# Kernel optimization log

Hardware: AMD Instinct MI355X
Metric: run time of the kernel (lower is better)

## Reference

```python
import jax, jax.numpy as jnp
import numpy as np

ADMP = 8  # admp_channel -> K = ADMP*ADMP keypoints


def setup_inputs() -> dict:
    key = jax.random.key(0)
    kA, kB = jax.random.split(key)
    B, C, H, W = 8, 512, 96, 96
    feature_A = jax.random.normal(kA, (B, C, H, W), dtype=jnp.float32)
    feature_B = jax.random.normal(kB, (B, C, H, W), dtype=jnp.float32)
    return {"feature_A": feature_A, "feature_B": feature_B}


def _keypoint_rowcol(feature_A):
    # featureSelect: sum over channels, AdaptiveMaxPool2d(ADMP) with return_indices.
    # H,W divisible by ADMP so adaptive pool == uniform non-overlapping pooling.
    B, C, H, W = feature_A.shape
    ph, pw = H // ADMP, W // ADMP
    resp = feature_A.sum(axis=1)  # [B,H,W]
    r = resp.reshape(B, ADMP, ph, ADMP, pw).transpose(0, 1, 3, 2, 4)
    r = r.reshape(B, ADMP * ADMP, ph * pw)
    loc = jnp.argmax(r, axis=-1)  # first-max, matches torch  [B,K]
    kk = jnp.arange(ADMP * ADMP)
    gi, gj = kk // ADMP, kk % ADMP
    row_A = gi[None, :] * ph + loc // pw  # [B,K]
    col_A = gj[None, :] * pw + loc % pw
    return row_A, col_A


def reference(feature_A, feature_B):
    B, C, H, W = feature_A.shape
    K = ADMP * ADMP
    row_A, col_A = _keypoint_rowcol(feature_A)
    flat_A = row_A * W + col_A  # [B,K]

    # gather descriptors: [B,K,C]
    fa = feature_A.reshape(B, C, H * W)
    desc = jnp.take_along_axis(fa, flat_A[:, None, :], axis=2).transpose(0, 2, 1)

    # squared L2 distance map via ||b||^2 - 2 a.b + ||a||^2 : [B,K,HW]
    fb = feature_B.reshape(B, C, H * W)
    fb_sq = jnp.sum(fb * fb, axis=1)            # [B,HW]
    d_sq = jnp.sum(desc * desc, axis=-1)        # [B,K]
    cross = jnp.einsum('bkc,bcn->bkn', desc, fb)  # [B,K,HW]
    dist = fb_sq[:, None, :] - 2.0 * cross + d_sq[:, :, None]

    min_idx = jnp.argmin(dist, axis=-1)  # [B,K]
    row_B = min_idx // W
    col_B = min_idx % W
    drow = -(row_B - row_A)
    dcol = -(col_B - col_A)
    off = jnp.stack([drow, dcol], axis=-1)  # [B,K,2] int

    # getTranslationalOffsetByMode: most frequent (drow,dcol) pair per batch
    eq = jnp.all(off[:, :, None, :] == off[:, None, :, :], axis=-1)  # [B,K,K]
    counts = eq.sum(axis=-1)  # [B,K]
    best = jnp.argmax(counts, axis=-1)  # first occurrence on ties, matches dict order
    out = jnp.take_along_axis(off, best[:, None, None], axis=1)[:, 0, :]  # [B,2]
    return out
```

## Files before the change

### kernel.cpp

```cpp
#include <hip/hip_runtime.h>
#include <hip/hip_bf16.h>
#include <math.h>

typedef _Float16 half8 __attribute__((ext_vector_type(8)));
typedef __fp16 fp16x2 __attribute__((ext_vector_type(2)));
typedef float f32x4 __attribute__((ext_vector_type(4)));
typedef unsigned short u16x4 __attribute__((ext_vector_type(4)));
typedef unsigned short u16x8 __attribute__((ext_vector_type(8)));

#define B_   8
#define C_   512
#define H_   96
#define W_   96
#define HW   9216
#define K_   64
#define PH   12
#define PW   12
#define NT   96
#define CCH  32
#define NBLK 96

#define OFF_PARTIAL 0u
#define OFF_CANDV   0u
#define OFF_CANDN   294912u
#define OFF_DESCH   2359296u
#define OFF_DESCL   2883584u
#define OFF_ROWA    3407872u
#define OFF_COLA    3409920u

#define FBT_HI 0
#define FBT_LO 3072
#define DSC_HI 6144
#define DSC_LO 8704
#define BUFHW  11264

__global__ __launch_bounds__(256) void k_partial(const float* __restrict__ A,
                                                 float* __restrict__ part) {
    int idx4 = blockIdx.x * 256 + threadIdx.x;
    int chunk = blockIdx.y;
    int b = idx4 / (HW / 4), hw4 = idx4 - b * (HW / 4);
    const float* p = A + ((size_t)(b * C_ + chunk * 64)) * HW + hw4 * 4;
    float4 s = make_float4(0.f, 0.f, 0.f, 0.f);
#pragma unroll
    for (int i = 0; i < 64; ++i) {
        float4 v = *(const float4*)&p[(size_t)i * HW];
        s.x += v.x; s.y += v.y; s.z += v.z; s.w += v.w;
    }
    *(float4*)&part[chunk * (B_ * HW) + b * HW + hw4 * 4] = s;
}

__global__ void k_selgather(const float* __restrict__ part, const float* __restrict__ A,
                            int* __restrict__ rowA, int* __restrict__ colA,
                            _Float16* __restrict__ descH, _Float16* __restrict__ descL) {
    int k = blockIdx.x, b = blockIdx.y, lane = threadIdx.x;
    int gi = k >> 3, gj = k & 7;
    float bv = -1e30f; int bp = 1 << 20;
    for (int p = lane; p < PH * PW; p += 64) {
        int lr = p / PW, lc = p - lr * PW;
        int hw = (gi * PH + lr) * W_ + gj * PW + lc;
        float v = 0.f;
#pragma unroll
        for (int ch = 0; ch < 8; ++ch) v += part[ch * (B_ * HW) + b * HW + hw];
        if (v > bv || (v == bv && p < bp)) { bv = v; bp = p; }
    }
    for (int m = 1; m < 64; m <<= 1) {
        float ov = __shfl_xor(bv, m);
        int   op = __shfl_xor(bp, m);
        if (ov > bv || (ov == bv && op < bp)) { bv = ov; bp = op; }
    }
    int lr = bp / PW, lc = bp - lr * PW;
    int r = gi * PH + lr, c = gj * PW + lc;
    int flat = r * W_ + c;
    if (lane == 0) { rowA[b * K_ + k] = r; colA[b * K_ + k] = c; }
#pragma unroll
    for (int i = 0; i < 8; ++i) {
        int cc = i * 64 + lane;
        float v = A[((size_t)(b * C_ + cc)) * HW + flat];
        _Float16 h = (_Float16)v;
        _Float16 lo = (_Float16)((v - (float)h) * 2048.f);
        size_t o = ((size_t)(b * K_ + k)) * C_ + cc;
        descH[o] = h; descL[o] = lo;
    }
}

__global__ __launch_bounds__(256, 3) void k_main(const float* __restrict__ FB,
                                                 const _Float16* __restrict__ descH,
                                                 const _Float16* __restrict__ descL,
                                                 float* __restrict__ candV,
                                                 int* __restrict__ candN) {
    __shared__ __attribute__((aligned(16))) unsigned short smem_us[2 * BUFHW];
    int b = blockIdx.y, nb = blockIdx.x * NT;
    int tid = threadIdx.x;
    int l = tid & 63;
    int w = tid >> 6;
    const size_t baseB = (size_t)b * C_ * HW + nb;

    const int so = tid % 12;
    const int scb = tid / 12;
    const int st_nt = so >> 1, st_nn0 = (so & 1) * 8;
    const int dk = tid >> 2, dco = tid & 3;

    f32x4 accH[6], accX[6];
#pragma unroll
    for (int nt = 0; nt < 6; ++nt) {
        accH[nt] = (f32x4){0.f, 0.f, 0.f, 0.f};
        accX[nt] = (f32x4){0.f, 0.f, 0.f, 0.f};
    }
    float sq[8];
#pragma unroll
    for (int j = 0; j < 8; ++j) sq[j] = 0.f;

    float4 r0a, r0b, r1a, r1b;
    u16x8 rdH, rdL;

#define LOADFB(c0)                                                            \
    do {                                                                      \
        if (tid < 192) {                                                      \
            const float* p0 = &FB[baseB + (size_t)((c0) + scb) * HW + so * 8];      \
            const float* p1 = &FB[baseB + (size_t)((c0) + scb + 16) * HW + so * 8]; \
            r0a = *(const float4*)p0; r0b = *(const float4*)(p0 + 4);         \
            r1a = *(const float4*)p1; r1b = *(const float4*)(p1 + 4);         \
        }                                                                     \
    } while (0)

#define LOADDESC(c0)                                                          \
    do {                                                                      \
        size_t o = ((size_t)(b * K_) + dk) * C_ + (c0) + dco * 8;             \
        rdH = *(const u16x8*)&descH[o];                                       \
        rdL = *(const u16x8*)&descL[o];                                       \
    } while (0)

#define CVT8(va, vb, hofs)                                                    \
    do {                                                                      \
        union { fp16x2 p[4]; half8 h; } hh, ll;                               \
        float vv[8] = {va.x, va.y, va.z, va.w, vb.x, vb.y, vb.z, vb.w};       \
        _Pragma("unroll")                                                     \
        for (int j = 0; j < 4; ++j) {                                         \
            float a = vv[2 * j], bq = vv[2 * j + 1];                          \
            fp16x2 hp = __builtin_amdgcn_cvt_pkrtz(a, bq);                    \
            float ha = (float)hp[0], hb = (float)hp[1];                       \
            fp16x2 lp = __builtin_amdgcn_cvt_pkrtz((a - ha) * 2048.f,         \
                                                   (bq - hb) * 2048.f);       \
            hh.p[j] = hp; ll.p[j] = lp;                                       \
            sq[2 * j]     = fmaf(a, a, sq[2 * j]);                            \
            sq[2 * j + 1] = fmaf(bq, bq, sq[2 * j + 1]);                      \
        }                                                                     \
        *(half8*)&smem_us[(hofs)] = hh.h;                                     \
        *(half8*)&smem_us[(hofs) + FBT_LO] = ll.h;                            \
    } while (0)

#define WRITEFB(bufhw)                                                        \
    do {                                                                      \
        if (tid < 192) {                                                      \
            int c = scb;                                                      \
            int off0 = (bufhw) + FBT_HI + st_nt * 512 + ((c >> 2) & 1) * 256  \
                       + (c >> 3) * 64 + (c & 3) * 16 + st_nn0;               \
            CVT8(r0a, r0b, off0);                                             \
            c = scb + 16;                                                     \
            int off1 = (bufhw) + FBT_HI + st_nt * 512 + ((c >> 2) & 1) * 256  \
                       + (c >> 3) * 64 + (c & 3) * 16 + st_nn0;               \
            CVT8(r1a, r1b, off1);                                             \
        }                                                                     \
    } while (0)

#define WRITEDESC(bufhw)                                                      \
    do {                                                                      \
        *(u16x8*)&smem_us[(bufhw) + DSC_HI + dk * 40 + dco * 8] = rdH;        \
        *(u16x8*)&smem_us[(bufhw) + DSC_LO + dk * 40 + dco * 8] = rdL;        \
    } while (0)

    LOADFB(0);
    LOADDESC(0);
    WRITEFB(0);
    WRITEDESC(0);
    __syncthreads();

    const unsigned lds0 = (unsigned)(size_t)&smem_us[0];

#define TRQ(d0, d1, d2, d3, addr)                                             \
    asm volatile("ds_read_b64_tr_b16 %0, %1"             : "=v"(d0) : "v"(addr)); \
    asm volatile("ds_read_b64_tr_b16 %0, %1 offset:512"  : "=v"(d1) : "v"(addr)); \
    asm volatile("ds_read_b64_tr_b16 %0, %1 offset:6144" : "=v"(d2) : "v"(addr)); \
    asm volatile("ds_read_b64_tr_b16 %0, %1 offset:6656" : "=v"(d3) : "v"(addr));

#define WAIT4 asm volatile("s_waitcnt lgkmcnt(4)" ::: "memory");              \
              __builtin_amdgcn_sched_barrier(0);
#define WAIT0 asm volatile("s_waitcnt lgkmcnt(0)" ::: "memory");              \
              __builtin_amdgcn_sched_barrier(0);

#define MFMA3(nt, h0_, h1_, l0_, l1_)                                         \
    do {                                                                      \
        union { u16x4 q[2]; half8 h; } bh, bl;                                \
        bh.q[0] = h0_; bh.q[1] = h1_; bl.q[0] = l0_; bl.q[1] = l1_;           \
        accH[nt] = __builtin_amdgcn_mfma_f32_16x16x32_f16(aHu.h, bh.h, accH[nt], 0, 0, 0); \
        accX[nt] = __builtin_amdgcn_mfma_f32_16x16x32_f16(aHu.h, bl.h, accX[nt], 0, 0, 0); \
        accX[nt] = __builtin_amdgcn_mfma_f32_16x16x32_f16(aLu.h, bh.h, accX[nt], 0, 0, 0); \
    } while (0)

    for (int t = 0; t < 16; ++t) {
        const int cur = (t & 1) ? BUFHW : 0;
        const int nxt = BUFHW - cur;
        if (t < 15) { LOADFB((t + 1) * CCH); LOADDESC((t + 1) * CCH); }

        union { u16x8 u; half8 h; } aHu, aLu;
        const unsigned abase = lds0 +
            (unsigned)(cur + DSC_HI + (w * 16 + (l & 15)) * 40 + (l >> 4) * 8) * 2u;
        asm volatile("ds_read_b128 %0, %1"             : "=v"(aHu.u) : "v"(abase));
        asm volatile("ds_read_b128 %0, %1 offset:5120" : "=v"(aLu.u) : "v"(abase));
        const unsigned trb = lds0 + (unsigned)cur * 2u + (unsigned)l * 8u;
        u16x4 xh0, xh1, xl0, xl1, yh0, yh1, yl0, yl1;
        TRQ(xh0, xh1, xl0, xl1, trb);
        TRQ(yh0, yh1, yl0, yl1, trb + 1024u);
        WAIT4;
        MFMA3(0, xh0, xh1, xl0, xl1);
        TRQ(xh0, xh1, xl0, xl1, trb + 2048u);
        WAIT4;
        MFMA3(1, yh0, yh1, yl0, yl1);
        TRQ(yh0, yh1, yl0, yl1, trb + 3072u);
        WAIT4;
        MFMA3(2, xh0, xh1, xl0, xl1);
        TRQ(xh0, xh1, xl0, xl1, trb + 4096u);
        WAIT4;
        MFMA3(3, yh0, yh1, yl0, yl1);
        TRQ(yh0, yh1, yl0, yl1, trb + 5120u);
        WAIT4;
        MFMA3(4, xh0, xh1, xl0, xl1);
        WAIT0;
        MFMA3(5, yh0, yh1, yl0, yl1);

        if (t < 15) { WRITEFB(nxt); WRITEDESC(nxt); }
        __syncthreads();
    }

    float* fscr = (float*)&smem_us[0];
    if (tid < 192) {
        *(float4*)&fscr[scb * 96 + so * 8]     = make_float4(sq[0], sq[1], sq[2], sq[3]);
        *(float4*)&fscr[scb * 96 + so * 8 + 4] = make_float4(sq[4], sq[5], sq[6], sq[7]);
    }
    __syncthreads();
    if (tid < 96) {
        float s = 0.f;
#pragma unroll
        for (int g = 0; g < 16; ++g) s += fscr[g * 96 + tid];
        fscr[1536 + tid] = s;
    }
    __syncthreads();

    const float inv2048 = 1.f / 2048.f;
#pragma unroll
    for (int r = 0; r < 4; ++r) {
        float bv = 1e30f; int bn = 1 << 28;
#pragma unroll
        for (int nt = 0; nt < 6; ++nt) {
            float cross = accH[nt][r] + accX[nt][r] * inv2048;
            float d = fscr[1536 + nt * 16 + (l & 15)] - 2.f * cross;
            int n = nb + nt * 16 + (l & 15);
            if (d < bv) { bv = d; bn = n; }
        }
#pragma unroll
        for (int m = 1; m < 16; m <<= 1) {
            float ov = __shfl_xor(bv, m);
            int   on = __shfl_xor(bn, m);
            if (ov < bv || (ov == bv && on < bn)) { bv = ov; bn = on; }
        }
        if ((l & 15) == 0) {
            int k = w * 16 + (l >> 4) * 4 + r;
            candV[(b * K_ + k) * NBLK + blockIdx.x] = bv;
            candN[(b * K_ + k) * NBLK + blockIdx.x] = bn;
        }
    }
#undef LOADFB
#undef LOADDESC
#undef CVT8
#undef WRITEFB
#undef WRITEDESC
#undef TRQ
#undef WAIT4
#undef WAIT0
#undef MFMA3
}

__global__ void k_redmode(const float* __restrict__ candV, const int* __restrict__ candN,
                          const int* __restrict__ rowA, const int* __restrict__ colA,
                          int* __restrict__ out) {
    __shared__ int r_s[64], c_s[64];
    int b = blockIdx.x, k = threadIdx.x;
    int base = (b * K_ + k) * NBLK;
    float bv = 1e30f; int bn = 1 << 28;
    for (int j = 0; j < NBLK; ++j) {
        float ov = candV[base + j]; int on = candN[base + j];
        if (ov < bv || (ov == bv && on < bn)) { bv = ov; bn = on; }
    }
    int rB = bn / W_, cB = bn - rB * W_;
    r_s[k] = rowA[b * K_ + k] - rB;
    c_s[k] = colA[b * K_ + k] - cB;
    __syncthreads();
    int mr = r_s[k], mc = c_s[k], cnt = 0;
#pragma unroll
    for (int j = 0; j < 64; ++j) cnt += (r_s[j] == mr && c_s[j] == mc) ? 1 : 0;
    int bk = k, bc = cnt;
    for (int m = 1; m < 64; m <<= 1) {
        int oc = __shfl_xor(bc, m);
        int ok = __shfl_xor(bk, m);
        if (oc > bc || (oc == bc && ok < bk)) { bc = oc; bk = ok; }
    }
    if (k == 0) { out[b * 2] = r_s[bk]; out[b * 2 + 1] = c_s[bk]; }
}

extern "C" void kernel_launch(void* const* d_in, const int* in_sizes, int n_in,
                              void* d_out, int out_size, void* d_ws, size_t ws_size,
                              hipStream_t stream) {
    const float* A  = (const float*)d_in[0];
    const float* FB = (const float*)d_in[1];
    char* ws = (char*)d_ws;
    float*     part  = (float*)(ws + OFF_PARTIAL);
    _Float16*  descH = (_Float16*)(ws + OFF_DESCH);
    _Float16*  descL = (_Float16*)(ws + OFF_DESCL);
    int*       rowA  = (int*)(ws + OFF_ROWA);
    int*       colA  = (int*)(ws + OFF_COLA);
    float*     candV = (float*)(ws + OFF_CANDV);
    int*       candN = (int*)(ws + OFF_CANDN);
    int*       out   = (int*)d_out;

    k_partial<<<dim3((B_ * HW) / 1024, 8), 256, 0, stream>>>(A, part);
    k_selgather<<<dim3(K_, B_), 64, 0, stream>>>(part, A, rowA, colA, descH, descL);
    k_main<<<dim3(NBLK, B_), 256, 0, stream>>>(FB, descH, descL, candV, candN);
    k_redmode<<<dim3(B_), 64, 0, stream>>>(candV, candN, rowA, colA, out);
}
```

Before: 93.89 us.

## Prefetch global loads two chunks ahead with dual register sets and deeper LDS pipelining

Keeps two register sets (A/B) for feature_B and descriptor chunks so global loads are issued two iterations ahead instead of one. This hides more global memory latency behind the MFMA work. The loop is unrolled by two with alternating LDS buffers. The LDS transpose reads are deepened to three tiles in flight (waiting at lgkmcnt 8), and s_setprio raises wave priority during the compute phase. In exchange, register pressure rises and occupancy may drop.

Result: no change. 93.28 us (-0.6%).

```diff
diff --git a/kernel.cpp b/kernel.cpp
--- a/kernel.cpp
+++ b/kernel.cpp
@@ -110,24 +110,20 @@
 #pragma unroll
     for (int j = 0; j < 8; ++j) sq[j] = 0.f;
 
-    float4 r0a, r0b, r1a, r1b;
-    u16x8 rdH, rdL;
-
-#define LOADFB(c0)                                                            \
+    float4 Ar0a, Ar0b, Ar1a, Ar1b; u16x8 ArdH, ArdL;
+    float4 Br0a, Br0b, Br1a, Br1b; u16x8 BrdH, BrdL;
+
+#define LOADALL(S, c0)                                                        \
     do {                                                                      \
         if (tid < 192) {                                                      \
             const float* p0 = &FB[baseB + (size_t)((c0) + scb) * HW + so * 8];      \
             const float* p1 = &FB[baseB + (size_t)((c0) + scb + 16) * HW + so * 8]; \
-            r0a = *(const float4*)p0; r0b = *(const float4*)(p0 + 4);         \
-            r1a = *(const float4*)p1; r1b = *(const float4*)(p1 + 4);         \
+            S##r0a = *(const float4*)p0; S##r0b = *(const float4*)(p0 + 4);   \
+            S##r1a = *(const float4*)p1; S##r1b = *(const float4*)(p1 + 4);   \
         }                                                                     \
-    } while (0)
-
-#define LOADDESC(c0)                                                          \
-    do {                                                                      \
         size_t o = ((size_t)(b * K_) + dk) * C_ + (c0) + dco * 8;             \
-        rdH = *(const u16x8*)&descH[o];                                       \
-        rdL = *(const u16x8*)&descL[o];                                       \
+        S##rdH = *(const u16x8*)&descH[o];                                    \
+        S##rdL = *(const u16x8*)&descL[o];                                    \
     } while (0)
 
 #define CVT8(va, vb, hofs)                                                    \
@@ -149,31 +145,21 @@
         *(half8*)&smem_us[(hofs) + FBT_LO] = ll.h;                            \
     } while (0)
 
-#define WRITEFB(bufhw)                                                        \
+#define WRITEALL(S, bufhw)                                                    \
     do {                                                                      \
         if (tid < 192) {                                                      \
             int c = scb;                                                      \
             int off0 = (bufhw) + FBT_HI + st_nt * 512 + ((c >> 2) & 1) * 256  \
                        + (c >> 3) * 64 + (c & 3) * 16 + st_nn0;               \
-            CVT8(r0a, r0b, off0);                                             \
+            CVT8(S##r0a, S##r0b, off0);                                       \
             c = scb + 16;                                                     \
             int off1 = (bufhw) + FBT_HI + st_nt * 512 + ((c >> 2) & 1) * 256  \
                        + (c >> 3) * 64 + (c & 3) * 16 + st_nn0;               \
-            CVT8(r1a, r1b, off1);                                             \
+            CVT8(S##r1a, S##r1b, off1);                                       \
         }                                                                     \
-    } while (0)
-
-#define WRITEDESC(bufhw)                                                      \
-    do {                                                                      \
-        *(u16x8*)&smem_us[(bufhw) + DSC_HI + dk * 40 + dco * 8] = rdH;        \
-        *(u16x8*)&smem_us[(bufhw) + DSC_LO + dk * 40 + dco * 8] = rdL;        \
-    } while (0)
-
-    LOADFB(0);
-    LOADDESC(0);
-    WRITEFB(0);
-    WRITEDESC(0);
-    __syncthreads();
+        *(u16x8*)&smem_us[(bufhw) + DSC_HI + dk * 40 + dco * 8] = S##rdH;     \
+        *(u16x8*)&smem_us[(bufhw) + DSC_LO + dk * 40 + dco * 8] = S##rdL;     \
+    } while (0)
 
     const unsigned lds0 = (unsigned)(size_t)&smem_us[0];
 
@@ -183,6 +169,8 @@
     asm volatile("ds_read_b64_tr_b16 %0, %1 offset:6144" : "=v"(d2) : "v"(addr)); \
     asm volatile("ds_read_b64_tr_b16 %0, %1 offset:6656" : "=v"(d3) : "v"(addr));
 
+#define WAIT8 asm volatile("s_waitcnt lgkmcnt(8)" ::: "memory");              \
+              __builtin_amdgcn_sched_barrier(0);
 #define WAIT4 asm volatile("s_waitcnt lgkmcnt(4)" ::: "memory");              \
               __builtin_amdgcn_sched_barrier(0);
 #define WAIT0 asm volatile("s_waitcnt lgkmcnt(0)" ::: "memory");              \
@@ -197,38 +185,52 @@
         accX[nt] = __builtin_amdgcn_mfma_f32_16x16x32_f16(aLu.h, bh.h, accX[nt], 0, 0, 0); \
     } while (0)
 
-    for (int t = 0; t < 16; ++t) {
-        const int cur = (t & 1) ? BUFHW : 0;
-        const int nxt = BUFHW - cur;
-        if (t < 15) { LOADFB((t + 1) * CCH); LOADDESC((t + 1) * CCH); }
-
-        union { u16x8 u; half8 h; } aHu, aLu;
-        const unsigned abase = lds0 +
-            (unsigned)(cur + DSC_HI + (w * 16 + (l & 15)) * 40 + (l >> 4) * 8) * 2u;
-        asm volatile("ds_read_b128 %0, %1"             : "=v"(aHu.u) : "v"(abase));
-        asm volatile("ds_read_b128 %0, %1 offset:5120" : "=v"(aLu.u) : "v"(abase));
-        const unsigned trb = lds0 + (unsigned)cur * 2u + (unsigned)l * 8u;
-        u16x4 xh0, xh1, xl0, xl1, yh0, yh1, yl0, yl1;
-        TRQ(xh0, xh1, xl0, xl1, trb);
-        TRQ(yh0, yh1, yl0, yl1, trb + 1024u);
-        WAIT4;
-        MFMA3(0, xh0, xh1, xl0, xl1);
-        TRQ(xh0, xh1, xl0, xl1, trb + 2048u);
-        WAIT4;
-        MFMA3(1, yh0, yh1, yl0, yl1);
-        TRQ(yh0, yh1, yl0, yl1, trb + 3072u);
-        WAIT4;
-        MFMA3(2, xh0, xh1, xl0, xl1);
-        TRQ(xh0, xh1, xl0, xl1, trb + 4096u);
-        WAIT4;
-        MFMA3(3, yh0, yh1, yl0, yl1);
-        TRQ(yh0, yh1, yl0, yl1, trb + 5120u);
-        WAIT4;
-        MFMA3(4, xh0, xh1, xl0, xl1);
-        WAIT0;
-        MFMA3(5, yh0, yh1, yl0, yl1);
-
-        if (t < 15) { WRITEFB(nxt); WRITEDESC(nxt); }
+#define COMPUTE(cur)                                                          \
+    do {                                                                      \
+        union { u16x8 u; half8 h; } aHu, aLu;                                 \
+        const unsigned abase = lds0 +                                         \
+            (unsigned)((cur) + DSC_HI + (w * 16 + (l & 15)) * 40 + (l >> 4) * 8) * 2u; \
+        __builtin_amdgcn_s_setprio(1);                                        \
+        asm volatile("ds_read_b128 %0, %1"             : "=v"(aHu.u) : "v"(abase)); \
+        asm volatile("ds_read_b128 %0, %1 offset:5120" : "=v"(aLu.u) : "v"(abase)); \
+        const unsigned trb = lds0 + (unsigned)(cur) * 2u + (unsigned)l * 8u;  \
+        u16x4 xh0, xh1, xl0, xl1, yh0, yh1, yl0, yl1, zh0, zh1, zl0, zl1;     \
+        TRQ(xh0, xh1, xl0, xl1, trb);                                 \
+        TRQ(yh0, yh1, yl0, yl1, trb + 1024u);                         \
+        TRQ(zh0, zh1, zl0, zl1, trb + 2048u);                         \
+        WAIT8;                                              \
+        MFMA3(0, xh0, xh1, xl0, xl1);                                         \
+        TRQ(xh0, xh1, xl0, xl1, trb + 3072u);                         \
+        WAIT8;                                                  \
+        MFMA3(1, yh0, yh1, yl0, yl1);                                         \
+        TRQ(yh0, yh1, yl0, yl1, trb + 4096u);                         \
+        WAIT8;                                                  \
+        MFMA3(2, zh0, zh1, zl0, zl1);                                         \
+        TRQ(zh0, zh1, zl0, zl1, trb + 5120u);                         \
+        WAIT8;                                                  \
+        MFMA3(3, xh0, xh1, xl0, xl1);                                         \
+        WAIT4;                                                  \
+        MFMA3(4, yh0, yh1, yl0, yl1);                                         \
+        WAIT0;                                                  \
+        MFMA3(5, zh0, zh1, zl0, zl1);                                         \
+        __builtin_amdgcn_s_setprio(0);                                        \
+    } while (0)
+
+    LOADALL(A, 0);
+    WRITEALL(A, 0);
+    LOADALL(B, CCH);
+    __syncthreads();
+
+#pragma unroll 1
+    for (int tp = 0; tp < 8; ++tp) {
+        const int t0 = 2 * tp, t1 = 2 * tp + 1;
+        if (t0 + 2 < 16) LOADALL(A, (t0 + 2) * CCH);
+        COMPUTE(0);
+        if (t0 + 1 < 16) WRITEALL(B, BUFHW);
+        __syncthreads();
+        if (t1 + 2 < 16) LOADALL(B, (t1 + 2) * CCH);
+        COMPUTE(BUFHW);
+        if (t1 + 1 < 16) WRITEALL(A, 0);
         __syncthreads();
     }
 
@@ -269,15 +271,15 @@
             candN[(b * K_ + k) * NBLK + blockIdx.x] = bn;
         }
     }
-#undef LOADFB
-#undef LOADDESC
+#undef LOADALL
 #undef CVT8
-#undef WRITEFB
-#undef WRITEDESC
+#undef WRITEALL
 #undef TRQ
+#undef WAIT8
 #undef WAIT4
 #undef WAIT0
 #undef MFMA3
+#undef COMPUTE
 }
 
 __global__ void k_redmode(const float* __restrict__ candV, const int* __restrict__ candN,
```

## Retile distance GEMM to 64-column tiles with register-held descriptors and double-buffered loads

Applied to the files above, without the earlier changes.

The main GEMM kernel now processes 64 spatial columns per block with 64-channel chunks, giving 144 blocks per batch instead of 96. Descriptor fragments are loaded straight from global memory into registers instead of being staged through LDS. The two feature-B register sets are alternated so the next chunk's loads overlap the current MFMAs, and s_setprio is raised around the compute. Occupancy is targeted at 4 blocks per CU and k_partial uses 128-thread blocks. The larger candidate array adds reduction work, and the extra register buffers may pressure the occupancy target.

Result: slower. 149.1 us (+58.8%).

```diff
diff --git a/kernel.cpp b/kernel.cpp
--- a/kernel.cpp
+++ b/kernel.cpp
@@ -16,9 +16,9 @@
 #define K_   64
 #define PH   12
 #define PW   12
-#define NT   96
-#define CCH  32
-#define NBLK 96
+#define NT   64
+#define CCH  64
+#define NBLK 144
 
 #define OFF_PARTIAL 0u
 #define OFF_CANDV   0u
@@ -28,15 +28,12 @@
 #define OFF_ROWA    3407872u
 #define OFF_COLA    3409920u
 
-#define FBT_HI 0
-#define FBT_LO 3072
-#define DSC_HI 6144
-#define DSC_LO 8704
-#define BUFHW  11264
-
-__global__ __launch_bounds__(256) void k_partial(const float* __restrict__ A,
+#define FBT_LO 4096
+#define BUFHW  8192
+
+__global__ __launch_bounds__(128) void k_partial(const float* __restrict__ A,
                                                  float* __restrict__ part) {
-    int idx4 = blockIdx.x * 256 + threadIdx.x;
+    int idx4 = blockIdx.x * 128 + threadIdx.x;
     int chunk = blockIdx.y;
     int b = idx4 / (HW / 4), hw4 = idx4 - b * (HW / 4);
     const float* p = A + ((size_t)(b * C_ + chunk * 64)) * HW + hw4 * 4;
@@ -83,7 +80,7 @@
     }
 }
 
-__global__ __launch_bounds__(256, 3) void k_main(const float* __restrict__ FB,
+__global__ __launch_bounds__(256, 4) void k_main(const float* __restrict__ FB,
                                                  const _Float16* __restrict__ descH,
                                                  const _Float16* __restrict__ descL,
                                                  float* __restrict__ candV,
@@ -95,14 +92,15 @@
     int w = tid >> 6;
     const size_t baseB = (size_t)b * C_ * HW + nb;
 
-    const int so = tid % 12;
-    const int scb = tid / 12;
-    const int st_nt = so >> 1, st_nn0 = (so & 1) * 8;
-    const int dk = tid >> 2, dco = tid & 3;
-
-    f32x4 accH[6], accX[6];
-#pragma unroll
-    for (int nt = 0; nt < 6; ++nt) {
+    const int o_ = tid & 7;
+    const int cr = tid >> 3;
+    const int nt_ = o_ >> 1, oct_ = o_ & 1;
+    const int stb = nt_ * 1024 + ((cr >> 2) & 1) * 256 + (cr >> 3) * 64
+                    + (cr & 3) * 16 + oct_ * 8;
+
+    f32x4 accH[4], accX[4];
+#pragma unroll
+    for (int nt = 0; nt < 4; ++nt) {
         accH[nt] = (f32x4){0.f, 0.f, 0.f, 0.f};
         accX[nt] = (f32x4){0.f, 0.f, 0.f, 0.f};
     }
@@ -110,24 +108,25 @@
 #pragma unroll
     for (int j = 0; j < 8; ++j) sq[j] = 0.f;
 
-    float4 r0a, r0b, r1a, r1b;
-    u16x8 rdH, rdL;
-
-#define LOADFB(c0)                                                            \
-    do {                                                                      \
-        if (tid < 192) {                                                      \
-            const float* p0 = &FB[baseB + (size_t)((c0) + scb) * HW + so * 8];      \
-            const float* p1 = &FB[baseB + (size_t)((c0) + scb + 16) * HW + so * 8]; \
-            r0a = *(const float4*)p0; r0b = *(const float4*)(p0 + 4);         \
-            r1a = *(const float4*)p1; r1b = *(const float4*)(p1 + 4);         \
-        }                                                                     \
+    float4 Aa0, Aa1, Ab0, Ab1;
+    float4 Ba0, Ba1, Bb0, Bb1;
+    u16x8 dH0, dH1, dL0, dL1;
+
+#define LOADFB(S, c0)                                                         \
+    do {                                                                      \
+        const float* p0 = &FB[baseB + (size_t)((c0) + cr) * HW + o_ * 8];     \
+        S##a0 = *(const float4*)p0; S##a1 = *(const float4*)(p0 + 4);         \
+        const float* p1 = &FB[baseB + (size_t)((c0) + cr + 32) * HW + o_ * 8];\
+        S##b0 = *(const float4*)p1; S##b1 = *(const float4*)(p1 + 4);         \
     } while (0)
 
 #define LOADDESC(c0)                                                          \
     do {                                                                      \
-        size_t o = ((size_t)(b * K_) + dk) * C_ + (c0) + dco * 8;             \
-        rdH = *(const u16x8*)&descH[o];                                       \
-        rdL = *(const u16x8*)&descL[o];                                       \
+        size_t o = ((size_t)(b * K_) + w * 16 + (l & 15)) * C_ + (c0) + (l >> 4) * 8; \
+        dH0 = *(const u16x8*)&descH[o];                                       \
+        dH1 = *(const u16x8*)&descH[o + 32];                                  \
+        dL0 = *(const u16x8*)&descL[o];                                       \
+        dL1 = *(const u16x8*)&descL[o + 32];                                  \
     } while (0)
 
 #define CVT8(va, vb, hofs)                                                    \
@@ -149,100 +148,89 @@
         *(half8*)&smem_us[(hofs) + FBT_LO] = ll.h;                            \
     } while (0)
 
-#define WRITEFB(bufhw)                                                        \
-    do {                                                                      \
-        if (tid < 192) {                                                      \
-            int c = scb;                                                      \
-            int off0 = (bufhw) + FBT_HI + st_nt * 512 + ((c >> 2) & 1) * 256  \
-                       + (c >> 3) * 64 + (c & 3) * 16 + st_nn0;               \
-            CVT8(r0a, r0b, off0);                                             \
-            c = scb + 16;                                                     \
-            int off1 = (bufhw) + FBT_HI + st_nt * 512 + ((c >> 2) & 1) * 256  \
-                       + (c >> 3) * 64 + (c & 3) * 16 + st_nn0;               \
-            CVT8(r1a, r1b, off1);                                             \
-        }                                                                     \
-    } while (0)
-
-#define WRITEDESC(bufhw)                                                      \
-    do {                                                                      \
-        *(u16x8*)&smem_us[(bufhw) + DSC_HI + dk * 40 + dco * 8] = rdH;        \
-        *(u16x8*)&smem_us[(bufhw) + DSC_LO + dk * 40 + dco * 8] = rdL;        \
-    } while (0)
-
-    LOADFB(0);
-    LOADDESC(0);
-    WRITEFB(0);
-    WRITEDESC(0);
-    __syncthreads();
+#define WRITEFB(S, bufhw)                                                     \
+    do {                                                                      \
+        CVT8(S##a0, S##a1, (bufhw) + stb);            \
+        CVT8(S##b0, S##b1, (bufhw) + stb + 512);      \
+    } while (0)
 
     const unsigned lds0 = (unsigned)(size_t)&smem_us[0];
 
 #define TRQ(d0, d1, d2, d3, addr)                                             \
     asm volatile("ds_read_b64_tr_b16 %0, %1"             : "=v"(d0) : "v"(addr)); \
     asm volatile("ds_read_b64_tr_b16 %0, %1 offset:512"  : "=v"(d1) : "v"(addr)); \
-    asm volatile("ds_read_b64_tr_b16 %0, %1 offset:6144" : "=v"(d2) : "v"(addr)); \
-    asm volatile("ds_read_b64_tr_b16 %0, %1 offset:6656" : "=v"(d3) : "v"(addr));
+    asm volatile("ds_read_b64_tr_b16 %0, %1 offset:8192" : "=v"(d2) : "v"(addr)); \
+    asm volatile("ds_read_b64_tr_b16 %0, %1 offset:8704" : "=v"(d3) : "v"(addr));
 
 #define WAIT4 asm volatile("s_waitcnt lgkmcnt(4)" ::: "memory");              \
               __builtin_amdgcn_sched_barrier(0);
 #define WAIT0 asm volatile("s_waitcnt lgkmcnt(0)" ::: "memory");              \
               __builtin_amdgcn_sched_barrier(0);
 
-#define MFMA3(nt, h0_, h1_, l0_, l1_)                                         \
+#define MFMA3(nt, AH, AL, h0_, h1_, l0_, l1_)                                 \
     do {                                                                      \
         union { u16x4 q[2]; half8 h; } bh, bl;                                \
+        union { u16x8 u; half8 h; } ah, al;                                   \
         bh.q[0] = h0_; bh.q[1] = h1_; bl.q[0] = l0_; bl.q[1] = l1_;           \
-        accH[nt] = __builtin_amdgcn_mfma_f32_16x16x32_f16(aHu.h, bh.h, accH[nt], 0, 0, 0); \
-        accX[nt] = __builtin_amdgcn_mfma_f32_16x16x32_f16(aHu.h, bl.h, accX[nt], 0, 0, 0); \
-        accX[nt] = __builtin_amdgcn_mfma_f32_16x16x32_f16(aLu.h, bh.h, accX[nt], 0, 0, 0); \
-    } while (0)
-
-    for (int t = 0; t < 16; ++t) {
-        const int cur = (t & 1) ? BUFHW : 0;
-        const int nxt = BUFHW - cur;
-        if (t < 15) { LOADFB((t + 1) * CCH); LOADDESC((t + 1) * CCH); }
-
-        union { u16x8 u; half8 h; } aHu, aLu;
-        const unsigned abase = lds0 +
-            (unsigned)(cur + DSC_HI + (w * 16 + (l & 15)) * 40 + (l >> 4) * 8) * 2u;
-        asm volatile("ds_read_b128 %0, %1"             : "=v"(aHu.u) : "v"(abase));
-        asm volatile("ds_read_b128 %0, %1 offset:5120" : "=v"(aLu.u) : "v"(abase));
-        const unsigned trb = lds0 + (unsigned)cur * 2u + (unsigned)l * 8u;
-        u16x4 xh0, xh1, xl0, xl1, yh0, yh1, yl0, yl1;
-        TRQ(xh0, xh1, xl0, xl1, trb);
-        TRQ(yh0, yh1, yl0, yl1, trb + 1024u);
-        WAIT4;
-        MFMA3(0, xh0, xh1, xl0, xl1);
-        TRQ(xh0, xh1, xl0, xl1, trb + 2048u);
-        WAIT4;
-        MFMA3(1, yh0, yh1, yl0, yl1);
-        TRQ(yh0, yh1, yl0, yl1, trb + 3072u);
-        WAIT4;
-        MFMA3(2, xh0, xh1, xl0, xl1);
-        TRQ(xh0, xh1, xl0, xl1, trb + 4096u);
-        WAIT4;
-        MFMA3(3, yh0, yh1, yl0, yl1);
-        TRQ(yh0, yh1, yl0, yl1, trb + 5120u);
-        WAIT4;
-        MFMA3(4, xh0, xh1, xl0, xl1);
-        WAIT0;
-        MFMA3(5, yh0, yh1, yl0, yl1);
-
-        if (t < 15) { WRITEFB(nxt); WRITEDESC(nxt); }
+        ah.u = AH; al.u = AL;                                                 \
+        accH[nt] = __builtin_amdgcn_mfma_f32_16x16x32_f16(ah.h, bh.h, accH[nt], 0, 0, 0); \
+        accX[nt] = __builtin_amdgcn_mfma_f32_16x16x32_f16(ah.h, bl.h, accX[nt], 0, 0, 0); \
+        accX[nt] = __builtin_amdgcn_mfma_f32_16x16x32_f16(al.h, bh.h, accX[nt], 0, 0, 0); \
+    } while (0)
+
+#define COMPUTE(curhw)                                                        \
+    do {                                                                      \
+        const unsigned trb = lds0 + (unsigned)(curhw) * 2u + (unsigned)l * 8u;\
+        u16x4 xh0, xh1, xl0, xl1, yh0, yh1, yl0, yl1;                         \
+        __builtin_amdgcn_s_setprio(1);                                        \
+        TRQ(xh0, xh1, xl0, xl1, trb);                          \
+        TRQ(yh0, yh1, yl0, yl1, trb + 2048u);                  \
+        WAIT4; MFMA3(0, dH0, dL0, xh0, xh1, xl0, xl1);                        \
+        TRQ(xh0, xh1, xl0, xl1, trb + 4096u);                  \
+        WAIT4; MFMA3(1, dH0, dL0, yh0, yh1, yl0, yl1);                        \
+        TRQ(yh0, yh1, yl0, yl1, trb + 6144u);                  \
+        WAIT4; MFMA3(2, dH0, dL0, xh0, xh1, xl0, xl1);                        \
+        TRQ(xh0, xh1, xl0, xl1, trb + 1024u);                  \
+        WAIT4; MFMA3(3, dH0, dL0, yh0, yh1, yl0, yl1);                        \
+        TRQ(yh0, yh1, yl0, yl1, trb + 3072u);                  \
+        WAIT4; MFMA3(0, dH1, dL1, xh0, xh1, xl0, xl1);                        \
+        TRQ(xh0, xh1, xl0, xl1, trb + 5120u);                  \
+        WAIT4; MFMA3(1, dH1, dL1, yh0, yh1, yl0, yl1);                        \
+        TRQ(yh0, yh1, yl0, yl1, trb + 7168u);                  \
+        WAIT4; MFMA3(2, dH1, dL1, xh0, xh1, xl0, xl1);                        \
+        WAIT0; MFMA3(3, dH1, dL1, yh0, yh1, yl0, yl1);                        \
+        __builtin_amdgcn_s_setprio(0);                                        \
+    } while (0)
+
+    LOADFB(A, 0);
+    LOADDESC(0);
+    WRITEFB(A, 0);
+    LOADFB(B, CCH);
+    __syncthreads();
+
+#pragma unroll 1
+    for (int tp = 0; tp < 4; ++tp) {
+        const int t0 = 2 * tp, t1 = 2 * tp + 1;
+        if (t0 + 2 < 8) LOADFB(A, (t0 + 2) * CCH);
+        COMPUTE(0);
+        LOADDESC(t1 * CCH);
+        WRITEFB(B, BUFHW);
         __syncthreads();
+        if (t1 + 2 < 8) LOADFB(B, (t1 + 2) * CCH);
+        COMPUTE(BUFHW);
+        if (t1 + 1 < 8) { LOADDESC((t1 + 1) * CCH); WRITEFB(A, 0); }
+        __syncthreads();
     }
 
     float* fscr = (float*)&smem_us[0];
-    if (tid < 192) {
-        *(float4*)&fscr[scb * 96 + so * 8]     = make_float4(sq[0], sq[1], sq[2], sq[3]);
-        *(float4*)&fscr[scb * 96 + so * 8 + 4] = make_float4(sq[4], sq[5], sq[6], sq[7]);
-    }
+    *(float4*)&fscr[cr * 64 + o_ * 8]     = make_float4(sq[0], sq[1], sq[2], sq[3]);
+    *(float4*)&fscr[cr * 64 + o_ * 8 + 4] = make_float4(sq[4], sq[5], sq[6], sq[7]);
     __syncthreads();
-    if (tid < 96) {
+    if (tid < 64) {
         float s = 0.f;
 #pragma unroll
-        for (int g = 0; g < 16; ++g) s += fscr[g * 96 + tid];
-        fscr[1536 + tid] = s;
+        for (int g = 0; g < 32; ++g) s += fscr[g * 64 + tid];
+        fscr[2048 + tid] = s;
     }
     __syncthreads();
 
@@ -251,9 +239,9 @@
     for (int r = 0; r < 4; ++r) {
         float bv = 1e30f; int bn = 1 << 28;
 #pragma unroll
-        for (int nt = 0; nt < 6; ++nt) {
+        for (int nt = 0; nt < 4; ++nt) {
             float cross = accH[nt][r] + accX[nt][r] * inv2048;
-            float d = fscr[1536 + nt * 16 + (l & 15)] - 2.f * cross;
+            float d = fscr[2048 + nt * 16 + (l & 15)] - 2.f * cross;
             int n = nb + nt * 16 + (l & 15);
             if (d < bv) { bv = d; bn = n; }
         }
@@ -273,11 +261,11 @@
 #undef LOADDESC
 #undef CVT8
 #undef WRITEFB
-#undef WRITEDESC
 #undef TRQ
 #undef WAIT4
 #undef WAIT0
 #undef MFMA3
+#undef COMPUTE
 }
 
 __global__ void k_redmode(const float* __restrict__ candV, const int* __restrict__ candN,
@@ -322,7 +310,7 @@
     int*       candN = (int*)(ws + OFF_CANDN);
     int*       out   = (int*)d_out;
 
-    k_partial<<<dim3((B_ * HW) / 1024, 8), 256, 0, stream>>>(A, part);
+    k_partial<<<dim3((B_ * HW) / 512, 8), 128, 0, stream>>>(A, part);
     k_selgather<<<dim3(K_, B_), 64, 0, stream>>>(part, A, rowA, colA, descH, descL);
     k_main<<<dim3(NBLK, B_), 256, 0, stream>>>(FB, descH, descL, candV, candN);
     k_redmode<<<dim3(B_), 64, 0, stream>>>(candV, candN, rowA, colA, out);
```
